# Kernel optimization log

Hardware: AMD Instinct MI355X
Metric: run time of the kernel (lower is better)

## Reference

```python
import jax, jax.numpy as jnp
import numpy as np

D_MODEL = 1024
D_STATE = 16
D_CONV = 4
EXPAND = 2
D_INNER = D_MODEL * EXPAND          # 2048
DT_RANK = max(1, D_MODEL // 16)     # 64
BATCH, SEQ = 4, 2048


def setup_inputs() -> dict:
    key = jax.random.key(0)
    ks = jax.random.split(key, 8)
    s = lambda n: 1.0 / np.sqrt(n)
    x = jax.random.normal(ks[0], (BATCH, SEQ, D_MODEL), jnp.float32)
    in_proj_w = jax.random.normal(ks[1], (2 * D_INNER, D_MODEL), jnp.float32) * s(D_MODEL)
    conv_w = jax.random.normal(ks[2], (D_INNER, 1, D_CONV), jnp.float32) * s(D_CONV)
    conv_b = jax.random.normal(ks[3], (D_INNER,), jnp.float32) * 0.01
    x_proj_w = jax.random.normal(ks[4], (DT_RANK + 2 * D_STATE, D_INNER), jnp.float32) * s(D_INNER)
    dt_proj_w = jax.random.normal(ks[5], (D_INNER, DT_RANK), jnp.float32) * s(DT_RANK)
    dt_proj_b = jax.random.normal(ks[6], (D_INNER,), jnp.float32) * 0.01
    A_log = jnp.broadcast_to(jnp.log(jnp.arange(1, D_STATE + 1, dtype=jnp.float32))[None, :],
                             (D_INNER, D_STATE)).copy()
    D_param = jnp.ones((D_INNER,), jnp.float32)
    out_proj_w = jax.random.normal(ks[7], (D_MODEL, D_INNER), jnp.float32) * s(D_INNER)
    return {"x": x, "in_proj_w": in_proj_w, "conv_w": conv_w, "conv_b": conv_b,
            "x_proj_w": x_proj_w, "dt_proj_w": dt_proj_w, "dt_proj_b": dt_proj_b,
            "A_log": A_log, "D_param": D_param, "out_proj_w": out_proj_w}


def _ssm_forward(x, in_proj_w, conv_w, conv_b, x_proj_w, dt_proj_w, dt_proj_b,
                 A_log, D_param, out_proj_w):
    B, L, _ = x.shape
    # input projection -> (B, L, 2*D_INNER), split into x_ssm and gate z
    xz = jnp.einsum('bld,ed->ble', x, in_proj_w)
    x_ssm, z = xz[..., :D_INNER], xz[..., D_INNER:]
    # causal depthwise conv1d (torch pads both sides then slices [:L] == left pad only)
    xc = jnp.transpose(x_ssm, (0, 2, 1))  # (B, D_INNER, L)
    xc = jax.lax.conv_general_dilated(
        xc, conv_w, window_strides=(1,), padding=[(D_CONV - 1, 0)],
        dimension_numbers=('NCH', 'OIH', 'NCH'), feature_group_count=D_INNER)
    xc = xc + conv_b[None, :, None]
    x_ssm = jax.nn.silu(jnp.transpose(xc, (0, 2, 1)))  # (B, L, D_INNER)
    # input-dependent dt, B, C
    dbl = jnp.einsum('bld,ed->ble', x_ssm, x_proj_w)  # (B, L, DT_RANK+2N)
    dt_x = dbl[..., :DT_RANK]
    B_x = dbl[..., DT_RANK:DT_RANK + D_STATE]
    C_x = dbl[..., DT_RANK + D_STATE:]
    dt = jax.nn.softplus(jnp.einsum('blr,dr->bld', dt_x, dt_proj_w) + dt_proj_b)  # (B, L, D_INNER)
    A = -jnp.exp(A_log)  # (D_INNER, D_STATE)

    # selective scan over L with lax.scan; carry h: (B, D_INNER, D_STATE)
    def step(h, inp):
        dt_t, B_t, C_t, x_t = inp  # (B,D), (B,N), (B,N), (B,D)
        dA = jnp.exp(dt_t[:, :, None] * A[None, :, :])          # (B, D, N)
        dB = dt_t[:, :, None] * B_t[:, None, :]                 # (B, D, N)
        h = dA * h + dB * x_t[:, :, None]
        y_t = jnp.einsum('bdn,bn->bd', h, C_t)
        return h, y_t

    h0 = jnp.zeros((B, D_INNER, D_STATE), x.dtype)
    xs = (jnp.moveaxis(dt, 1, 0), jnp.moveaxis(B_x, 1, 0),
          jnp.moveaxis(C_x, 1, 0), jnp.moveaxis(x_ssm, 1, 0))
    _, ys = jax.lax.scan(step, h0, xs)          # ys: (L, B, D_INNER)
    y = jnp.moveaxis(ys, 0, 1) + D_param[None, None, :] * x_ssm
    y = y * jax.nn.silu(z)
    return jnp.einsum('ble,de->bld', y, out_proj_w)


def reference(x, in_proj_w, conv_w, conv_b, x_proj_w, dt_proj_w, dt_proj_b,
              A_log, D_param, out_proj_w):
    return _ssm_forward(x, in_proj_w, conv_w, conv_b, x_proj_w, dt_proj_w,
                        dt_proj_b, A_log, D_param, out_proj_w)
```

## Files before the change

### kernel.cpp

```cpp
#include <hip/hip_runtime.h>
#include <hip/hip_bf16.h>
#include <math.h>

#define D_MODEL 1024
#define D_STATE 16
#define D_CONV 4
#define D_INNER 2048
#define DT_RANK 64
#define BATCH 4
#define SEQ 2048
#define ML (BATCH * SEQ)
#define NCH 64
#define CL (SEQ / NCH)

typedef __attribute__((ext_vector_type(8))) short short8;
typedef __attribute__((ext_vector_type(8))) unsigned short u16x8;
typedef __attribute__((ext_vector_type(4))) float f32x4;

__device__ __forceinline__ float bf2f(unsigned short u) {
  union { unsigned int i; float f; } v;
  v.i = ((unsigned int)u) << 16;
  return v.f;
}
__device__ __forceinline__ unsigned short f2bf(float f) {
  union { float f; unsigned int i; } u;
  u.f = f;
  unsigned int r = u.i + 0x7fffu + ((u.i >> 16) & 1u);
  return (unsigned short)(r >> 16);
}
__device__ __forceinline__ unsigned int f2bf_pk(float a, float b) {
  union { __hip_bfloat162 h; unsigned int u; } cv;
  cv.h = __float22bfloat162_rn(make_float2(a, b));
  return cv.u;
}
template <bool BF>
__device__ __forceinline__ float ld1(const void* p, size_t i) {
  if constexpr (BF) return bf2f(((const unsigned short*)p)[i]);
  else return ((const float*)p)[i];
}
template <bool BF>
__device__ __forceinline__ void ld4(const void* p, size_t i, float o[4]) {
  if constexpr (BF) {
    ushort4 v = *(const ushort4*)((const unsigned short*)p + i);
    o[0] = bf2f(v.x); o[1] = bf2f(v.y); o[2] = bf2f(v.z); o[3] = bf2f(v.w);
  } else {
    float4 v = *(const float4*)((const float*)p + i);
    o[0] = v.x; o[1] = v.y; o[2] = v.z; o[3] = v.w;
  }
}

__device__ __forceinline__ void gl_lds16(const unsigned short* g,
                                         unsigned short* l) {
  __builtin_amdgcn_global_load_lds(
      (const __attribute__((address_space(1))) void*)g,
      (__attribute__((address_space(3))) void*)l, 16, 0, 0);
}

__global__ void detect_kernel(const unsigned int* __restrict__ xw, int* flag) {
  __shared__ int cnt;
  if (threadIdx.x == 0) cnt = 0;
  __syncthreads();
  unsigned int w = xw[threadIdx.x];
  unsigned int e = (w >> 7) & 0xffu;
  if (e < 100u || e > 145u) atomicAdd(&cnt, 1);
  __syncthreads();
  if (threadIdx.x == 0) flag[0] = (cnt < 32) ? 1 : 0;
}

#define CVT_N0 (ML * 1024)
#define CVT_N1 (4096 * 1024)
#define CVT_N2 (1024 * 2048)
#define CVT_N3 (2048 * 64)
#define CVT_N4 (128 * 2048)
#define CVT_E0 CVT_N0
#define CVT_E1 (CVT_E0 + CVT_N1)
#define CVT_E2 (CVT_E1 + CVT_N2)
#define CVT_E3 (CVT_E2 + CVT_N3)
#define CVT_E4 (CVT_E3 + CVT_N4)

__device__ __forceinline__ void cvt4(const void* in, size_t i,
                                     unsigned short* out, size_t o, int bf) {
  if (bf) {
    *(ushort4*)(out + o) = *(const ushort4*)((const unsigned short*)in + i);
  } else {
    float4 f = *(const float4*)((const float*)in + i);
    uint2 v;
    v.x = f2bf_pk(f.x, f.y);
    v.y = f2bf_pk(f.z, f.w);
    *(uint2*)(out + o) = v;
  }
}

__global__ __launch_bounds__(256) void cvt_all_kernel(
    const void* __restrict__ x, const void* __restrict__ ipw,
    const void* __restrict__ opw, const void* __restrict__ dtw,
    const void* __restrict__ xpw, unsigned short* __restrict__ x_bf,
    unsigned short* __restrict__ ipw_bf, unsigned short* __restrict__ opw_bf,
    unsigned short* __restrict__ dtw_bf, unsigned short* __restrict__ xpw_pad,
    const int* __restrict__ flag) {
  const int bf = *flag;
  const size_t g = (size_t)(blockIdx.x * 256 + threadIdx.x) * 4;
  if (g < CVT_E0) {
    cvt4(x, g, x_bf, g, bf);
  } else if (g < CVT_E1) {
    const size_t i = g - CVT_E0;
    cvt4(ipw, i, ipw_bf, i, bf);
  } else if (g < CVT_E2) {
    const size_t i = g - CVT_E1;
    cvt4(opw, i, opw_bf, i, bf);
  } else if (g < CVT_E3) {
    const size_t i = g - CVT_E2;
    cvt4(dtw, i, dtw_bf, i, bf);
  } else if (g < CVT_E4) {
    const size_t i = g - CVT_E3;
    const int row = (int)(i >> 11);
    if (row < 96) {
      cvt4(xpw, i, xpw_pad, i, bf);
    } else {
      ushort4 z = {0, 0, 0, 0};
      *(ushort4*)(xpw_pad + i) = z;
    }
  }
}

#define K1_LDA 1024
#define K1_NT 16

#define K1_STG(srcbase, lds, t_, h_)                                       \
  {                                                                        \
    const unsigned short* s_ =                                             \
        (srcbase) + (size_t)(h_) * (128 * K1_LDA) + (size_t)(t_) * 64;     \
    unsigned short* d_ = (lds) + (((t_) & 1) * 2 + (h_)) * 8192 + w * 512; \
    gl_lds16(s_, d_);                                                      \
    gl_lds16(s_ + 64 * K1_LDA, d_ + 4096);                                 \
  }

__global__ __launch_bounds__(512, 2) void gemm256_k1(
    const unsigned short* __restrict__ A,
    const unsigned short* __restrict__ B,
    unsigned short* __restrict__ C) {
  __shared__ unsigned short As[32768];
  __shared__ unsigned short Bs[32768];
  const int tid = threadIdx.x;
  const int l = tid & 63, w = tid >> 6;
  const int bid = blockIdx.x;
  const int swz = (bid & 7) * 64 + (bid >> 3);
  const int m0 = (swz >> 4) * 256, n0 = (swz & 15) * 256;
  const int row0 = tid >> 3;
  const int c0 = (tid & 7) ^ (row0 & 7);
  const unsigned short* aSrc = A + (size_t)(m0 + row0) * K1_LDA + c0 * 8;
  const unsigned short* bSrc = B + (size_t)(n0 + row0) * K1_LDA + c0 * 8;
  const int q = l >> 4, mr = l & 15;
  const int wm = w >> 2, wn = w & 3;

  K1_STG(aSrc, As, 0, 0);
  K1_STG(aSrc, As, 0, 1);
  K1_STG(bSrc, Bs, 0, 0);
  K1_STG(bSrc, Bs, 0, 1);
  K1_STG(bSrc, Bs, 1, 0);
  K1_STG(bSrc, Bs, 1, 1);
  K1_STG(aSrc, As, 1, 0);
  asm volatile("s_waitcnt vmcnt(6)" ::: "memory");
  asm volatile("s_barrier" ::: "memory");

  f32x4 acc[8][4] = {};
  for (int t = 0; t < K1_NT; ++t) {
    const int tb = (t & 1) * 2;
    short8 bfr[4][2];
#pragma unroll
    for (int ni = 0; ni < 4; ++ni)
#pragma unroll
      for (int kk = 0; kk < 2; ++kk) {
        const int r = (wn & 1) * 64 + ni * 16 + mr;
        const int c = kk * 4 + q;
        bfr[ni][kk] = *(const short8*)&Bs[(tb + (wn >> 1)) * 8192 + r * 64 +
                                          ((c ^ (r & 7)) * 8)];
      }
#pragma unroll
    for (int p = 0; p < 4; ++p) {
      short8 af[2][2];
#pragma unroll
      for (int i = 0; i < 2; ++i)
#pragma unroll
        for (int kk = 0; kk < 2; ++kk) {
          const int r = (2 * p + i) * 16 + mr;
          const int c = kk * 4 + q;
          af[i][kk] = *(const short8*)&As[(tb + wm) * 8192 + r * 64 +
                                          ((c ^ (r & 7)) * 8)];
        }
      if (p == 0) {
        if (t + 1 < K1_NT) K1_STG(aSrc, As, t + 1, 1);
      } else if (p == 1) {
        if (t + 2 < K1_NT) K1_STG(bSrc, Bs, t + 2, 0);
      } else if (p == 2) {
        if (t + 2 < K1_NT) K1_STG(bSrc, Bs, t + 2, 1);
      } else {
        if (t + 2 < K1_NT) K1_STG(aSrc, As, t + 2, 0);
      }
      asm volatile("s_barrier" ::: "memory");
      __builtin_amdgcn_s_setprio(1);
#pragma unroll
      for (int i = 0; i < 2; ++i)
#pragma unroll
        for (int ni = 0; ni < 4; ++ni)
#pragma unroll
          for (int kk = 0; kk < 2; ++kk)
            acc[2 * p + i][ni] = __builtin_amdgcn_mfma_f32_16x16x32_bf16(
                af[i][kk], bfr[ni][kk], acc[2 * p + i][ni], 0, 0, 0);
      __builtin_amdgcn_s_setprio(0);
      if (p == 3) {
        if (t + 2 < K1_NT) {
          asm volatile("s_waitcnt vmcnt(6)" ::: "memory");
        } else {
          asm volatile("s_waitcnt vmcnt(0)" ::: "memory");
        }
      }
      asm volatile("s_barrier" ::: "memory");
    }
  }
#pragma unroll
  for (int mi = 0; mi < 8; ++mi) {
#pragma unroll
    for (int ni = 0; ni < 4; ++ni) {
      const int row = m0 + wm * 128 + mi * 16 + q * 4;
      const int col = n0 + wn * 64 + ni * 16 + mr;
      const size_t off0 = (size_t)row * 4096 + col;
      const unsigned int p01 = f2bf_pk(acc[mi][ni][0], acc[mi][ni][1]);
      const unsigned int p23 = f2bf_pk(acc[mi][ni][2], acc[mi][ni][3]);
      C[off0] = (unsigned short)p01;
      C[off0 + 4096] = (unsigned short)(p01 >> 16);
      C[off0 + 2 * 4096] = (unsigned short)p23;
      C[off0 + 3 * 4096] = (unsigned short)(p23 >> 16);
    }
  }
}

__global__ __launch_bounds__(256) void dt_gemm_kernel(
    const unsigned short* __restrict__ Adbl,
    const unsigned short* __restrict__ Bw,
    unsigned short* __restrict__ Cdt,
    const void* __restrict__ bias, const int* __restrict__ flag) {
  __shared__ unsigned short Bs[128 * 64];
  __shared__ unsigned short Ass[4][128 * 64];
  const int tid = threadIdx.x;
  const int l = tid & 63, w = tid >> 6;
  const int bn = blockIdx.x * 128;
  const int mg = blockIdx.y * 512;
  const int srow = tid >> 3;
  const int sc = ((tid & 7) ^ (srow & 7)) * 8;
  const unsigned short* aSrc = Adbl + (size_t)(mg + srow) * 128 + sc;
  const unsigned short* bSrc = Bw + (size_t)(bn + srow) * 64 + sc;
#define K4_STGB(i_) gl_lds16(bSrc + (i_) * 32 * 64, Bs + (i_)*2048 + w * 512)
#define K4_STGA(mt_, i_)                                  \
  gl_lds16(aSrc + (size_t)((mt_)*128 + (i_)*32) * 128,    \
           Ass[(mt_) & 3] + (i_)*2048 + w * 512)
  K4_STGB(0); K4_STGB(1); K4_STGB(2); K4_STGB(3);
  K4_STGA(0, 0); K4_STGA(0, 1); K4_STGA(0, 2); K4_STGA(0, 3);
  K4_STGA(1, 0); K4_STGA(1, 1); K4_STGA(1, 2); K4_STGA(1, 3);
  asm volatile("s_waitcnt vmcnt(4)" ::: "memory");
  asm volatile("s_barrier" ::: "memory");
  const int q = l >> 4, mr = l & 15;
  const int wm = w >> 1, wn = w & 1;
  short8 bfr[4][2];
#pragma unroll
  for (int ni = 0; ni < 4; ++ni)
#pragma unroll
    for (int kk = 0; kk < 2; ++kk) {
      const int r = wn * 64 + ni * 16 + mr;
      const int c = kk * 4 + q;
      bfr[ni][kk] = *(const short8*)&Bs[r * 64 + ((c ^ (r & 7)) * 8)];
    }
  const int bf = *flag;
  float bv[4];
#pragma unroll
  for (int ni = 0; ni < 4; ++ni) {
    const int col = bn + wn * 64 + ni * 16 + mr;
    bv[ni] = bf ? ld1<true>(bias, col) : ld1<false>(bias, col);
  }
#pragma unroll
  for (int mt = 0; mt < 4; ++mt) {
    if (mt + 2 < 4) {
      K4_STGA(mt + 2, 0); K4_STGA(mt + 2, 1);
      K4_STGA(mt + 2, 2); K4_STGA(mt + 2, 3);
    }
    short8 af[4][2];
#pragma unroll
    for (int mi = 0; mi < 4; ++mi)
#pragma unroll
      for (int kk = 0; kk < 2; ++kk) {
        const int r = wm * 64 + mi * 16 + mr;
        const int c = kk * 4 + q;
        af[mi][kk] =
            *(const short8*)&Ass[mt & 3][r * 64 + ((c ^ (r & 7)) * 8)];
      }
    f32x4 acc[4][4] = {};
#pragma unroll
    for (int mi = 0; mi < 4; ++mi)
#pragma unroll
      for (int ni = 0; ni < 4; ++ni)
#pragma unroll
        for (int kk = 0; kk < 2; ++kk)
          acc[mi][ni] = __builtin_amdgcn_mfma_f32_16x16x32_bf16(
              af[mi][kk], bfr[ni][kk], acc[mi][ni], 0, 0, 0);
#pragma unroll
    for (int mi = 0; mi < 4; ++mi) {
#pragma unroll
      for (int ni = 0; ni < 4; ++ni) {
        const int row = mg + mt * 128 + wm * 64 + mi * 16 + q * 4;
        const int col = bn + wn * 64 + ni * 16 + mr;
        const size_t off0 = (size_t)row * 4096 + col;
        float v[4];
#pragma unroll
        for (int j = 0; j < 4; ++j) {
          const float t = acc[mi][ni][j] + bv[ni];
          v[j] = fmaxf(t, 0.f) + __logf(1.f + __expf(-fabsf(t)));
        }
        const unsigned int p01 = f2bf_pk(v[0], v[1]);
        const unsigned int p23 = f2bf_pk(v[2], v[3]);
        Cdt[off0] = (unsigned short)p01;
        Cdt[off0 + 4096] = (unsigned short)(p01 >> 16);
        Cdt[off0 + 2 * 4096] = (unsigned short)p23;
        Cdt[off0 + 3 * 4096] = (unsigned short)(p23 >> 16);
      }
    }
    if (mt + 2 < 4) {
      asm volatile("s_waitcnt vmcnt(4)" ::: "memory");
    } else {
      asm volatile("s_waitcnt vmcnt(0)" ::: "memory");
    }
    if (mt < 3) asm volatile("s_barrier" ::: "memory");
  }
}

template <int EPI, int TAG>
__global__ __launch_bounds__(256) void gemm_mfma(
    const unsigned short* __restrict__ Ain, int lda,
    const unsigned short* __restrict__ Bin, int ldb, void* __restrict__ C,
    int ldc, int K, const void* __restrict__ bias,
    const int* __restrict__ flag) {
  __shared__ unsigned short As[128 * 32];
  __shared__ unsigned short Bs[128 * 32];
  const unsigned short* A = Ain;
  const unsigned short* B = Bin;
  if (EPI == 3) {
    A += (size_t)blockIdx.z * 512;
    B += (size_t)blockIdx.z * 512;
  }
  const int tid = threadIdx.x;
  const int l = tid & 63, w = tid >> 6;
  const int bm = blockIdx.y * 128;
  const int bn = blockIdx.x * 128;
  const int r0 = w * 16 + (l >> 2);
  const int cc = (((l & 3) ^ ((l >> 2) & 3) ^ ((l >> 4) & 3))) * 8;
  const unsigned short* Ap0 = A + (size_t)(bm + r0) * lda + cc;
  const unsigned short* Ap1 = A + (size_t)(bm + r0 + 64) * lda + cc;
  const unsigned short* Bp0 = B + (size_t)(bn + r0) * ldb + cc;
  const unsigned short* Bp1 = B + (size_t)(bn + r0 + 64) * ldb + cc;
  const int q = l >> 4, mr = l & 15;
  const int wm = w >> 1, wn = w & 1;
  const int slot = (q ^ (mr & 3) ^ (mr >> 2)) * 8;
  f32x4 acc[4][4] = {};
  for (int k0 = 0; k0 < K; k0 += 32) {
    gl_lds16(Ap0 + k0, As + w * 512);
    gl_lds16(Ap1 + k0, As + 2048 + w * 512);
    gl_lds16(Bp0 + k0, Bs + w * 512);
    gl_lds16(Bp1 + k0, Bs + 2048 + w * 512);
    __syncthreads();
    short8 af[4], bfr[4];
#pragma unroll
    for (int mi = 0; mi < 4; ++mi)
      af[mi] = *(const short8*)&As[(wm * 64 + mi * 16 + mr) * 32 + slot];
#pragma unroll
    for (int ni = 0; ni < 4; ++ni)
      bfr[ni] = *(const short8*)&Bs[(wn * 64 + ni * 16 + mr) * 32 + slot];
#pragma unroll
    for (int mi = 0; mi < 4; ++mi)
#pragma unroll
      for (int ni = 0; ni < 4; ++ni)
        acc[mi][ni] = __builtin_amdgcn_mfma_f32_16x16x32_bf16(
            af[mi], bfr[ni], acc[mi][ni], 0, 0, 0);
    __syncthreads();
  }
  const int bf = (EPI == 1) ? *flag : 0;
  float* Cp3 = (EPI == 3)
                   ? ((float*)C + (size_t)blockIdx.z * ML * 128)
                   : (float*)C;
#pragma unroll
  for (int mi = 0; mi < 4; ++mi) {
#pragma unroll
    for (int ni = 0; ni < 4; ++ni) {
      const int row = bm + wm * 64 + mi * 16 + q * 4;
      const int col = bn + wn * 64 + ni * 16 + mr;
      const size_t off0 = (size_t)row * ldc + col;
      if (EPI == 0) {
        const unsigned int p01 = f2bf_pk(acc[mi][ni][0], acc[mi][ni][1]);
        const unsigned int p23 = f2bf_pk(acc[mi][ni][2], acc[mi][ni][3]);
        unsigned short* C16 = (unsigned short*)C;
        C16[off0] = (unsigned short)p01;
        C16[off0 + ldc] = (unsigned short)(p01 >> 16);
        C16[off0 + 2 * (size_t)ldc] = (unsigned short)p23;
        C16[off0 + 3 * (size_t)ldc] = (unsigned short)(p23 >> 16);
      } else if (EPI == 3) {
#pragma unroll
        for (int j = 0; j < 4; ++j)
          Cp3[off0 + (size_t)j * ldc] = acc[mi][ni][j];
      } else {
        if (bf) {
          const unsigned int p01 = f2bf_pk(acc[mi][ni][0], acc[mi][ni][1]);
          const unsigned int p23 = f2bf_pk(acc[mi][ni][2], acc[mi][ni][3]);
          unsigned short* C16 = (unsigned short*)C;
          C16[off0] = (unsigned short)p01;
          C16[off0 + ldc] = (unsigned short)(p01 >> 16);
          C16[off0 + 2 * (size_t)ldc] = (unsigned short)p23;
          C16[off0 + 3 * (size_t)ldc] = (unsigned short)(p23 >> 16);
        } else {
          float* Cf = (float*)C;
#pragma unroll
          for (int j = 0; j < 4; ++j)
            Cf[off0 + (size_t)j * ldc] = acc[mi][ni][j];
        }
      }
    }
  }
}

__global__ __launch_bounds__(256) void reduceK3_kernel(
    const float* __restrict__ part, unsigned short* __restrict__ dbl) {
  const size_t i = (size_t)(blockIdx.x * 256 + threadIdx.x) * 4;
  const size_t st = (size_t)ML * 128;
  float4 a = *(const float4*)(part + i);
  float4 b = *(const float4*)(part + st + i);
  float4 c = *(const float4*)(part + 2 * st + i);
  float4 d = *(const float4*)(part + 3 * st + i);
  uint2 v;
  v.x = f2bf_pk(a.x + b.x + c.x + d.x, a.y + b.y + c.y + d.y);
  v.y = f2bf_pk(a.z + b.z + c.z + d.z, a.w + b.w + c.w + d.w);
  *(uint2*)(dbl + i) = v;
}

__global__ __launch_bounds__(256) void conv_silu_kernel(
    const unsigned short* __restrict__ xzb, const void* __restrict__ cw,
    const void* __restrict__ cb, unsigned short* __restrict__ xcb,
    const int* __restrict__ flag) {
  const int bf = *flag;
  const int e = (blockIdx.x * 256 + threadIdx.x) * 4;
  const int d = e & (D_INNER - 1);
  const int bl = e >> 11;
  const int l = bl & (SEQ - 1);
  const size_t base = (size_t)bl * 4096 + d;
  float x0[4], x1[4] = {}, x2[4] = {}, x3[4] = {};
  ld4<true>(xzb, base, x0);
  if (l >= 1) ld4<true>(xzb, base - 4096, x1);
  if (l >= 2) ld4<true>(xzb, base - 2 * 4096, x2);
  if (l >= 3) ld4<true>(xzb, base - 3 * 4096, x3);
  float r[4];
#pragma unroll
  for (int i = 0; i < 4; ++i) {
    float w[4];
    if (bf) ld4<true>(cw, (size_t)(d + i) * 4, w);
    else ld4<false>(cw, (size_t)(d + i) * 4, w);
    const float bias = bf ? ld1<true>(cb, d + i) : ld1<false>(cb, d + i);
    float acc = bias + w[3] * x0[i] + w[2] * x1[i] + w[1] * x2[i] + w[0] * x3[i];
    r[i] = acc / (1.f + __expf(-acc));
  }
  uint2 o;
  o.x = f2bf_pk(r[0], r[1]);
  o.y = f2bf_pk(r[2], r[3]);
  *(uint2*)(xcb + e) = o;
}

__device__ __forceinline__ void load_a(const void* A_log, int bf, int d,
                                       float a[16], float& dev) {
  float t[4];
#pragma unroll
  for (int k = 0; k < 4; ++k) {
    if (bf) ld4<true>(A_log, (size_t)d * 16 + k * 4, t);
    else ld4<false>(A_log, (size_t)d * 16 + k * 4, t);
#pragma unroll
    for (int j = 0; j < 4; ++j) a[k * 4 + j] = -expf(t[j]);
  }
  dev = 0.f;
#pragma unroll
  for (int n = 0; n < 16; ++n) dev = fmaxf(dev, fabsf(a[n] + (float)(n + 1)));
}

__device__ __forceinline__ void pow_tree(float e1, float pw[16]) {
  const float e2 = e1 * e1;
  const float e3 = e2 * e1;
  const float e4 = e2 * e2;
  pw[0] = e1; pw[1] = e2; pw[2] = e3; pw[3] = e4;
  pw[4] = e4 * e1; pw[5] = e4 * e2; pw[6] = e4 * e3; pw[7] = e4 * e4;
  const float e8 = pw[7];
  pw[8] = e8 * e1; pw[9] = e8 * e2; pw[10] = e8 * e3; pw[11] = e8 * e4;
  pw[12] = e8 * pw[4]; pw[13] = e8 * pw[5]; pw[14] = e8 * pw[6];
  pw[15] = e8 * e8;
}

__global__ __launch_bounds__(256) void scan_passA(
    const unsigned short* __restrict__ xzb,
    const unsigned short* __restrict__ xcb,
    const unsigned short* __restrict__ dbl, const void* __restrict__ A_log,
    const int* __restrict__ flag, float* __restrict__ S,
    float* __restrict__ P) {
  const int bf = *flag;
  const int gid = blockIdx.x * 256 + threadIdx.x;
  const int d = gid & (D_INNER - 1);
  const int c = (gid >> 11) & (NCH - 1);
  const int b = gid >> 17;
  float a[16], dev;
  load_a(A_log, bf, d, a, dev);
  float h[16] = {};
  float sdt = 0.f;
  const size_t m0 = (size_t)b * SEQ + c * CL;
  if (dev < 1e-3f) {
    for (int t = 0; t < CL; ++t) {
      const size_t m = m0 + t;
      const float dtv = bf2f(xzb[m * 4096 + d]);
      const float xv = bf2f(xcb[m * 2048 + d]);
      const u16x8 B0 = *(const u16x8*)&dbl[m * 128 + 64];
      const u16x8 B1 = *(const u16x8*)&dbl[m * 128 + 72];
      const float dtx = dtv * xv;
      sdt += dtv;
      float pw[16];
      pow_tree(__expf(-dtv), pw);
#pragma unroll
      for (int n = 0; n < 16; ++n) {
        const float Bv = bf2f(n < 8 ? B0[n] : B1[n - 8]);
        h[n] = fmaf(pw[n], h[n], Bv * dtx);
      }
    }
  } else {
    for (int t = 0; t < CL; ++t) {
      const size_t m = m0 + t;
      const float dtv = bf2f(xzb[m * 4096 + d]);
      const float xv = bf2f(xcb[m * 2048 + d]);
      const u16x8 B0 = *(const u16x8*)&dbl[m * 128 + 64];
      const u16x8 B1 = *(const u16x8*)&dbl[m * 128 + 72];
      const float dtx = dtv * xv;
      sdt += dtv;
#pragma unroll
      for (int n = 0; n < 16; ++n) {
        const float Bv = bf2f(n < 8 ? B0[n] : B1[n - 8]);
        h[n] = fmaf(__expf(dtv * a[n]), h[n], Bv * dtx);
      }
    }
  }
  const size_t sidx = (((size_t)b * NCH + c) * D_INNER + d) * 16;
#pragma unroll
  for (int n = 0; n < 16; ++n) {
    S[sidx + n] = h[n];
    P[sidx + n] = __expf(a[n] * sdt);
  }
}

__global__ __launch_bounds__(256) void scan_passB(float* __restrict__ S,
                                                  const float* __restrict__ P) {
  const int idx = blockIdx.x * 256 + threadIdx.x;
  const int n = idx & 15;
  const int d = (idx >> 4) & (D_INNER - 1);
  const int b = idx >> 15;
  float h = 0.f;
  for (int c = 0; c < NCH; ++c) {
    const size_t sidx = (((size_t)b * NCH + c) * D_INNER + d) * 16 + n;
    const float s = S[sidx], p = P[sidx];
    S[sidx] = h;
    h = p * h + s;
  }
}

__global__ __launch_bounds__(256) void scan_passC(
    const unsigned short* __restrict__ xzb,
    const unsigned short* __restrict__ xcb,
    const unsigned short* __restrict__ dbl, const void* __restrict__ A_log,
    const void* __restrict__ Dp, const float* __restrict__ S,
    const int* __restrict__ flag, unsigned short* __restrict__ ybf) {
  const int bf = *flag;
  const int gid = blockIdx.x * 256 + threadIdx.x;
  const int d = gid & (D_INNER - 1);
  const int c = (gid >> 11) & (NCH - 1);
  const int b = gid >> 17;
  float a[16], dev;
  load_a(A_log, bf, d, a, dev);
  const float Dv = bf ? ld1<true>(Dp, d) : ld1<false>(Dp, d);
  float h[16];
  const size_t sidx = (((size_t)b * NCH + c) * D_INNER + d) * 16;
#pragma unroll
  for (int n = 0; n < 16; ++n) h[n] = S[sidx + n];
  const size_t m0 = (size_t)b * SEQ + c * CL;
  const bool trick = dev < 1e-3f;
  for (int t = 0; t < CL; ++t) {
    const size_t m = m0 + t;
    const float dtv = bf2f(xzb[m * 4096 + d]);
    const float xv = bf2f(xcb[m * 2048 + d]);
    const u16x8 B0 = *(const u16x8*)&dbl[m * 128 + 64];
    const u16x8 B1 = *(const u16x8*)&dbl[m * 128 + 72];
    const u16x8 C0 = *(const u16x8*)&dbl[m * 128 + 80];
    const u16x8 C1 = *(const u16x8*)&dbl[m * 128 + 88];
    const float dtx = dtv * xv;
    float y = 0.f;
    if (trick) {
      float pw[16];
      pow_tree(__expf(-dtv), pw);
#pragma unroll
      for (int n = 0; n < 16; ++n) {
        const float Bv = bf2f(n < 8 ? B0[n] : B1[n - 8]);
        const float Cv = bf2f(n < 8 ? C0[n] : C1[n - 8]);
        h[n] = fmaf(pw[n], h[n], Bv * dtx);
        y = fmaf(h[n], Cv, y);
      }
    } else {
#pragma unroll
      for (int n = 0; n < 16; ++n) {
        const float Bv = bf2f(n < 8 ? B0[n] : B1[n - 8]);
        const float Cv = bf2f(n < 8 ? C0[n] : C1[n - 8]);
        h[n] = fmaf(__expf(dtv * a[n]), h[n], Bv * dtx);
        y = fmaf(h[n], Cv, y);
      }
    }
    const float zv = bf2f(xzb[m * 4096 + 2048 + d]);
    const float yv = y + Dv * xv;
    ybf[m * 2048 + d] = f2bf(yv * (zv / (1.f + __expf(-zv))));
  }
}

extern "C" void kernel_launch(void* const* d_in, const int* in_sizes, int n_in,
                              void* d_out, int out_size, void* d_ws,
                              size_t ws_size, hipStream_t stream) {
  const void* x = d_in[0];
  const void* in_proj_w = d_in[1];
  const void* conv_w = d_in[2];
  const void* conv_b = d_in[3];
  const void* x_proj_w = d_in[4];
  const void* dt_proj_w = d_in[5];
  const void* dt_proj_b = d_in[6];
  const void* A_log = d_in[7];
  const void* D_param = d_in[8];
  const void* out_proj_w = d_in[9];

  char* wsb = (char*)d_ws;
  int* flag = (int*)wsb;
  unsigned short* xzb = (unsigned short*)(wsb + 256);
  unsigned short* xcb = xzb + (size_t)ML * 4096;
  unsigned short* dbl = xcb + (size_t)ML * 2048;
  unsigned short* ybf = dbl + (size_t)ML * 128;
  float* S = (float*)(ybf + (size_t)ML * 2048);
  float* P = S + (size_t)BATCH * NCH * D_INNER * 16;
  unsigned short* opw_bf =
      (unsigned short*)(P + (size_t)BATCH * NCH * D_INNER * 16);
  unsigned short* xpw_pad = opw_bf + (size_t)1024 * 2048;
  unsigned short* dtw_bf = xpw_pad + (size_t)128 * 2048;
  unsigned short* x_bf = xcb;
  unsigned short* ipw_bf = xcb + (size_t)ML * 1024;
  float* k3part = S;

  detect_kernel<<<1, 256, 0, stream>>>((const unsigned int*)x, flag);
  cvt_all_kernel<<<CVT_E4 / 1024, 256, 0, stream>>>(
      x, in_proj_w, out_proj_w, dt_proj_w, x_proj_w, x_bf, ipw_bf, opw_bf,
      dtw_bf, xpw_pad, flag);
  gemm256_k1<<<dim3(512), 512, 0, stream>>>(x_bf, ipw_bf, xzb);
  conv_silu_kernel<<<(ML * D_INNER) / 1024, 256, 0, stream>>>(
      xzb, conv_w, conv_b, xcb, flag);
  {
    dim3 g(1, ML / 128, 4);
    gemm_mfma<3, 3><<<g, 256, 0, stream>>>(xcb, 2048, xpw_pad, 2048, k3part,
                                           128, 512, nullptr, flag);
  }
  reduceK3_kernel<<<(ML * 128) / 1024, 256, 0, stream>>>(k3part, dbl);
  dt_gemm_kernel<<<dim3(16, 16), 256, 0, stream>>>(dbl, dtw_bf, xzb,
                                                   dt_proj_b, flag);
  scan_passA<<<(BATCH * NCH * D_INNER) / 256, 256, 0, stream>>>(
      xzb, xcb, dbl, A_log, flag, S, P);
  scan_passB<<<(BATCH * D_INNER * 16) / 256, 256, 0, stream>>>(S, P);
  scan_passC<<<(BATCH * NCH * D_INNER) / 256, 256, 0, stream>>>(
      xzb, xcb, dbl, A_log, D_param, S, flag, ybf);
  {
    dim3 g(1024 / 128, ML / 128);
    gemm_mfma<1, 6><<<g, 256, 0, stream>>>(ybf, 2048, opw_bf, 2048, d_out,
                                           1024, 2048, nullptr, flag);
  }
}
```

Before: 484.1 us.

## Replace out_proj GEMM with dedicated 256x128 pipelined MFMA kernel

Adds a specialized out-projection GEMM kernel that uses 256x128 tiles with 512 threads, double-buffered LDS staging via direct global-to-LDS loads, and interleaves prefetch of later K-tiles with the MFMA work. It also sets wave priority around the MFMA bursts and remaps block IDs for L2 locality. The generic 128x128 gemm_mfma launch for out_proj is replaced. This is meant to improve data reuse and overlap of loads with compute, at the cost of higher LDS and register pressure and fewer blocks (256) on the device.

```diff
diff --git a/kernel.cpp b/kernel.cpp
--- a/kernel.cpp
+++ b/kernel.cpp
@@ -235,6 +235,131 @@
   }
 }
 
+#define K6_LDA 2048
+#define K6_NT 32
+
+#define K6_STGA(t_, h_)                                                 \
+  {                                                                     \
+    const unsigned short* s_ =                                          \
+        aSrc + (size_t)(h_) * (128 * K6_LDA) + (size_t)(t_) * 64;       \
+    unsigned short* d_ = As + (((t_) & 1) * 2 + (h_)) * 8192 + w * 512; \
+    gl_lds16(s_, d_);                                                   \
+    gl_lds16(s_ + 64 * K6_LDA, d_ + 4096);                              \
+  }
+#define K6_STGB(t_)                                            \
+  {                                                            \
+    const unsigned short* s_ = bSrc + (size_t)(t_) * 64;       \
+    unsigned short* d_ = Bs6 + ((t_) & 1) * 8192 + w * 512;    \
+    gl_lds16(s_, d_);                                          \
+    gl_lds16(s_ + 64 * K6_LDA, d_ + 4096);                     \
+  }
+
+__global__ __launch_bounds__(512, 2) void gemm256x128_k6(
+    const unsigned short* __restrict__ A,
+    const unsigned short* __restrict__ B,
+    void* __restrict__ C,
+    const int* __restrict__ flag) {
+  __shared__ unsigned short As[32768];
+  __shared__ unsigned short Bs6[16384];
+  const int tid = threadIdx.x;
+  const int l = tid & 63, w = tid >> 6;
+  const int bid = blockIdx.x;
+  const int swz = (bid & 7) * 32 + (bid >> 3);
+  const int n0 = (swz & 7) * 128, m0 = (swz >> 3) * 256;
+  const int row0 = tid >> 3;
+  const int c0 = (tid & 7) ^ (row0 & 7);
+  const unsigned short* aSrc = A + (size_t)(m0 + row0) * K6_LDA + c0 * 8;
+  const unsigned short* bSrc = B + (size_t)(n0 + row0) * K6_LDA + c0 * 8;
+  const int q = l >> 4, mr = l & 15;
+  const int wm = w >> 2, wn = w & 3;
+
+  K6_STGA(0, 0);
+  K6_STGA(0, 1);
+  K6_STGB(0);
+  K6_STGB(1);
+  K6_STGA(1, 0);
+  asm volatile("s_waitcnt vmcnt(4)" ::: "memory");
+  asm volatile("s_barrier" ::: "memory");
+
+  f32x4 acc[8][2] = {};
+  for (int t = 0; t < K6_NT; ++t) {
+    const int tb = (t & 1) * 2;
+    short8 bfr[2][2];
+#pragma unroll
+    for (int ni = 0; ni < 2; ++ni)
+#pragma unroll
+      for (int kk = 0; kk < 2; ++kk) {
+        const int r = wn * 32 + ni * 16 + mr;
+        const int c = kk * 4 + q;
+        bfr[ni][kk] = *(const short8*)&Bs6[(t & 1) * 8192 + r * 64 +
+                                           ((c ^ (r & 7)) * 8)];
+      }
+#pragma unroll
+    for (int p = 0; p < 4; ++p) {
+      short8 af[2][2];
+#pragma unroll
+      for (int i = 0; i < 2; ++i)
+#pragma unroll
+        for (int kk = 0; kk < 2; ++kk) {
+          const int r = (2 * p + i) * 16 + mr;
+          const int c = kk * 4 + q;
+          af[i][kk] = *(const short8*)&As[(tb + wm) * 8192 + r * 64 +
+                                          ((c ^ (r & 7)) * 8)];
+        }
+      if (p == 0) {
+        if (t + 1 < K6_NT) K6_STGA(t + 1, 1);
+      } else if (p == 1) {
+        if (t + 2 < K6_NT) K6_STGB(t + 2);
+      } else if (p == 3) {
+        if (t + 2 < K6_NT) K6_STGA(t + 2, 0);
+      }
+      asm volatile("s_barrier" ::: "memory");
+      __builtin_amdgcn_s_setprio(1);
+#pragma unroll
+      for (int i = 0; i < 2; ++i)
+#pragma unroll
+        for (int ni = 0; ni < 2; ++ni)
+#pragma unroll
+          for (int kk = 0; kk < 2; ++kk)
+            acc[2 * p + i][ni] = __builtin_amdgcn_mfma_f32_16x16x32_bf16(
+                af[i][kk], bfr[ni][kk], acc[2 * p + i][ni], 0, 0, 0);
+      __builtin_amdgcn_s_setprio(0);
+      if (p == 3) {
+        if (t + 2 < K6_NT) {
+          asm volatile("s_waitcnt vmcnt(4)" ::: "memory");
+        } else {
+          asm volatile("s_waitcnt vmcnt(0)" ::: "memory");
+        }
+      }
+      asm volatile("s_barrier" ::: "memory");
+    }
+  }
+  const int bf = *flag;
+#pragma unroll
+  for (int mi = 0; mi < 8; ++mi) {
+#pragma unroll
+    for (int ni = 0; ni < 2; ++ni) {
+      const int row = m0 + wm * 128 + mi * 16 + q * 4;
+      const int col = n0 + wn * 32 + ni * 16 + mr;
+      const size_t off0 = (size_t)row * 1024 + col;
+      if (bf) {
+        const unsigned int p01 = f2bf_pk(acc[mi][ni][0], acc[mi][ni][1]);
+        const unsigned int p23 = f2bf_pk(acc[mi][ni][2], acc[mi][ni][3]);
+        unsigned short* C16 = (unsigned short*)C;
+        C16[off0] = (unsigned short)p01;
+        C16[off0 + 1024] = (unsigned short)(p01 >> 16);
+        C16[off0 + 2 * 1024] = (unsigned short)p23;
+        C16[off0 + 3 * 1024] = (unsigned short)(p23 >> 16);
+      } else {
+        float* Cf = (float*)C;
+#pragma unroll
+        for (int j = 0; j < 4; ++j)
+          Cf[off0 + (size_t)j * 1024] = acc[mi][ni][j];
+      }
+    }
+  }
+}
+
 __global__ __launch_bounds__(256) void dt_gemm_kernel(
     const unsigned short* __restrict__ Adbl,
     const unsigned short* __restrict__ Bw,
@@ -673,9 +798,5 @@
   scan_passB<<<(BATCH * D_INNER * 16) / 256, 256, 0, stream>>>(S, P);
   scan_passC<<<(BATCH * NCH * D_INNER) / 256, 256, 0, stream>>>(
       xzb, xcb, dbl, A_log, D_param, S, flag, ybf);
-  {
-    dim3 g(1024 / 128, ML / 128);
-    gemm_mfma<1, 6><<<g, 256, 0, stream>>>(ybf, 2048, opw_bf, 2048, d_out,
-                                           1024, 2048, nullptr, flag);
-  }
-}
+  gemm256x128_k6<<<dim3(256), 512, 0, stream>>>(ybf, opw_bf, d_out, flag);
+}
```

New measurement: 472.5 us. 2.4% less time.
